# Kernel optimization log

Measured on AMD Instinct MI355X. Metric: run time of the kernel, lower is better.

## Reference

```python
import jax, jax.numpy as jnp
import numpy as np

B, S, H = 2, 2048, 1024
NH, NKV, HD = 16, 4, 64
G, R = NKV, NH // NKV  # 4 kv groups, 4 query heads per group


def setup_inputs() -> dict:
    key = jax.random.key(0)
    ks = jax.random.split(key, 7)
    scale = 1.0 / np.sqrt(H)
    return {
        "hidden_states": jax.random.normal(ks[0], (B, S, H), jnp.float32),
        "cos": jax.random.normal(ks[1], (S, HD), jnp.float32),
        "sin": jax.random.normal(ks[2], (S, HD), jnp.float32),
        "attention_mask": jnp.ones((B, S), jnp.float32),
        "Wq": jax.random.normal(ks[3], (H, NH * HD), jnp.float32) * scale,
        "Wk": jax.random.normal(ks[4], (H, NKV * HD), jnp.float32) * scale,
        "Wv": jax.random.normal(ks[5], (H, NKV * HD), jnp.float32) * scale,
        "Wo": jax.random.normal(ks[6], (NH * HD, H), jnp.float32) * scale,
    }


def _rotate_half(x):
    h = x.shape[-1] // 2
    return jnp.concatenate([-x[..., h:], x[..., :h]], axis=-1)


def reference(hidden_states, cos, sin, attention_mask, Wq, Wk, Wv, Wo):
    x = hidden_states
    q = (x @ Wq).reshape(B, S, NH, HD)
    k = (x @ Wk).reshape(B, S, NKV, HD)
    v = (x @ Wv).reshape(B, S, NKV, HD)
    # RoPE: cos/sin [S,HD] broadcast over batch and heads
    c = cos[None, :, None, :]
    s = sin[None, :, None, :]
    q = q * c + _rotate_half(q) * s
    k = k * c + _rotate_half(k) * s
    # GQA without materializing repeated KV: q grouped as [B,S,G,R,HD]
    qg = q.reshape(B, S, G, R, HD)
    scores = jnp.einsum("bsgrd,btgd->bgrst", qg, k) / np.sqrt(HD)  # [B,G,R,S,T]
    causal = jnp.tril(jnp.ones((S, S), bool))
    scores = jnp.where(causal[None, None, None], scores, -jnp.inf)
    scores = scores + ((1.0 - attention_mask) * -1e9)[:, None, None, None, :]
    probs = jax.nn.softmax(scores.astype(jnp.float32), axis=-1).astype(q.dtype)
    out = jnp.einsum("bgrst,btgd->bsgrd", probs, v).reshape(B, S, NH * HD)
    return out @ Wo
```

## Files before the change

kernel.cpp:

```cpp
#include <hip/hip_runtime.h>
#include <math.h>

#define B_   2
#define S_   2048
#define H_   1024
#define NH_  16
#define NKV_ 4
#define HD_  64
#define R_   (NH_ / NKV_)
#define QKVW 1536

typedef __attribute__((ext_vector_type(8))) short bf16x8;
typedef __attribute__((ext_vector_type(4))) float f32x4;

__device__ inline short f2bf(float f) {
    unsigned u = __float_as_uint(f);
    u += 0x7FFF + ((u >> 16) & 1);
    return (short)(u >> 16);
}

__device__ inline float exp2fast(float x) {
#if __has_builtin(__builtin_amdgcn_exp2f)
    return __builtin_amdgcn_exp2f(x);
#else
    float r; asm volatile("v_exp_f32 %0, %1\n\ts_nop 1" : "=v"(r) : "v"(x)); return r;
#endif
}

__device__ inline unsigned cvt_pk_bf16(float lo, float hi) {
    unsigned r;
    asm("v_cvt_pk_bf16_f32 %0, %1, %2" : "=v"(r) : "v"(lo), "v"(hi));
    return r;
}

#define LOG2E 1.4426950408889634f

__device__ inline void gload_lds16(const void* gptr, void* lptr) {
    __builtin_amdgcn_global_load_lds(
        (const __attribute__((address_space(1))) unsigned int*)gptr,
        (__attribute__((address_space(3))) unsigned int*)lptr,
        16, 0, 0);
}

__global__ __launch_bounds__(256) void tconv_all(const float* __restrict__ Wq,
                                                 const float* __restrict__ Wk,
                                                 const float* __restrict__ Wv,
                                                 const float* __restrict__ Wo,
                                                 short* __restrict__ Wqkvt,
                                                 short* __restrict__ Wot,
                                                 const float* __restrict__ x,
                                                 short* __restrict__ xb) {
    const int bx = blockIdx.x;
    const int tid = threadIdx.x;

    if (bx >= 640) {
        const size_t e0 = (size_t)(bx - 640) * 16384;
#pragma unroll
        for (int t = 0; t < 8; t++) {
            const size_t i = e0 + ((size_t)t * 256 + tid) * 8;
            float4 a = *(const float4*)&x[i];
            float4 c = *(const float4*)&x[i + 4];
            bf16x8 o;
            o[0] = f2bf(a.x); o[1] = f2bf(a.y); o[2] = f2bf(a.z); o[3] = f2bf(a.w);
            o[4] = f2bf(c.x); o[5] = f2bf(c.y); o[6] = f2bf(c.z); o[7] = f2bf(c.w);
            *(bf16x8*)&xb[i] = o;
        }
        return;
    }

    __shared__ short T[64][68];
    const float* W; short* Wt; int N, idx;
    if (bx < 256)      { W = Wq; Wt = Wqkvt;                     N = 1024; idx = bx; }
    else if (bx < 320) { W = Wk; Wt = Wqkvt + 1024 * 1024;       N = 256;  idx = bx - 256; }
    else if (bx < 384) { W = Wv; Wt = Wqkvt + 1280 * 1024;       N = 256;  idx = bx - 320; }
    else               { W = Wo; Wt = Wot;                       N = 1024; idx = bx - 384; }
    const int ntiles = N >> 6;
    const int n0 = (idx % ntiles) * 64;
    const int k0 = (idx / ntiles) * 64;

    const int r  = tid >> 4;
    const int c4 = (tid & 15) * 4;
#pragma unroll
    for (int t = 0; t < 4; t++) {
        int row = t * 16 + r;
        float4 v = *(const float4*)&W[(size_t)(k0 + row) * N + n0 + c4];
        T[c4 + 0][row] = f2bf(v.x);
        T[c4 + 1][row] = f2bf(v.y);
        T[c4 + 2][row] = f2bf(v.z);
        T[c4 + 3][row] = f2bf(v.w);
    }
    __syncthreads();
#pragma unroll
    for (int t = 0; t < 4; t++) {
        int row = t * 16 + r;
        short4 o = *(short4*)&T[row][c4];
        *(short4*)&Wt[(size_t)(n0 + row) * 1024 + k0 + c4] = o;
    }
}

__global__ __launch_bounds__(256) void gemm1_fused(const short* __restrict__ xb,
                                                   const short* __restrict__ Bt,
                                                   short* __restrict__ qkv,
                                                   short* __restrict__ Vtg,
                                                   const float* __restrict__ cosb,
                                                   const float* __restrict__ sinb) {
    __shared__ short Ah[2][64 * 32];
    __shared__ short Bh[2][128 * 32];

    const int tid  = threadIdx.x;
    const int w    = tid >> 6;
    const int lane = tid & 63;
    const int ln   = lane & 15;
    const int qd   = lane >> 4;
    const int wr   = w >> 1, wc = w & 1;
    const int row0 = blockIdx.y * 64;
    const int col0 = blockIdx.x * 128;

    const int sr = lane >> 2;
    const int sk = (lane & 3) * 8;

    const short* ap = xb + (size_t)(row0 + w * 16 + sr) * 1024 + sk;
    const short* bp0 = Bt + (size_t)(col0 + w * 32 + sr) * 1024 + sk;
    const short* bp1 = Bt + (size_t)(col0 + w * 32 + 16 + sr) * 1024 + sk;

    f32x4 acc[2][4];
#pragma unroll
    for (int mi = 0; mi < 2; mi++)
#pragma unroll
        for (int ni = 0; ni < 4; ni++)
            acc[mi][ni] = (f32x4){0.f, 0.f, 0.f, 0.f};

    gload_lds16(ap,  &Ah[0][(w * 16) * 32]);
    gload_lds16(bp0, &Bh[0][(w * 32) * 32]);
    gload_lds16(bp1, &Bh[0][(w * 32 + 16) * 32]);
    __syncthreads();

    for (int t = 0; t < 32; t++) {
        const int cur = t & 1, nxt = cur ^ 1;
        if (t + 1 < 32) {
            const int k1 = (t + 1) * 32;
            gload_lds16(ap + k1,  &Ah[nxt][(w * 16) * 32]);
            gload_lds16(bp0 + k1, &Bh[nxt][(w * 32) * 32]);
            gload_lds16(bp1 + k1, &Bh[nxt][(w * 32 + 16) * 32]);
        }

        bf16x8 af[2], bfr[4];
#pragma unroll
        for (int mi = 0; mi < 2; mi++)
            af[mi] = *(const bf16x8*)&Ah[cur][(wr * 32 + mi * 16 + ln) * 32 + qd * 8];
#pragma unroll
        for (int ni = 0; ni < 4; ni++)
            bfr[ni] = *(const bf16x8*)&Bh[cur][(wc * 64 + ni * 16 + ln) * 32 + qd * 8];
#pragma unroll
        for (int mi = 0; mi < 2; mi++)
#pragma unroll
            for (int ni = 0; ni < 4; ni++)
                acc[mi][ni] = __builtin_amdgcn_mfma_f32_16x16x32_bf16(af[mi], bfr[ni], acc[mi][ni], 0, 0, 0);

        __syncthreads();
    }

    const int colw = col0 + wc * 64;
    if (colw < H_ + NKV_ * HD_) {
#pragma unroll
        for (int mi = 0; mi < 2; mi++)
#pragma unroll
            for (int i = 0; i < 4; i++) {
                const int row  = row0 + wr * 32 + mi * 16 + qd * 4 + i;
                const int spos = row & (S_ - 1);
                const float* cp = cosb + (size_t)spos * HD_;
                const float* sp = sinb + (size_t)spos * HD_;
                float o0[4];
#pragma unroll
                for (int ni = 0; ni < 2; ni++) {
                    const int d = ni * 16 + ln;
                    float x0 = acc[mi][ni][i], x1 = acc[mi][ni + 2][i];
                    o0[ni]     = x0 * cp[d]      - x1 * sp[d];
                    o0[ni + 2] = x1 * cp[d + 32] + x0 * sp[d + 32];
                }
                short* Cp = qkv + (size_t)row * QKVW + colw + ln;
#pragma unroll
                for (int ni = 0; ni < 4; ni++) Cp[ni * 16] = f2bf(o0[ni]);
            }
    } else {
        const int g = (colw - (H_ + NKV_ * HD_)) >> 6;
#pragma unroll
        for (int mi = 0; mi < 2; mi++) {
            const int rbase = row0 + wr * 32 + mi * 16 + qd * 4;
            const int bg = ((rbase >> 11) * NKV_) + g;
            const int s0 = rbase & (S_ - 1);
#pragma unroll
            for (int ni = 0; ni < 4; ni++) {
                const int d = ni * 16 + ln;
                short4 pk = { f2bf(acc[mi][ni][0]), f2bf(acc[mi][ni][1]),
                              f2bf(acc[mi][ni][2]), f2bf(acc[mi][ni][3]) };
                *(short4*)&Vtg[((size_t)bg * HD_ + d) * S_ + s0] = pk;
            }
        }
    }
}

__global__ __launch_bounds__(256) void gemm2_bt(const short* __restrict__ A, int lda,
                                                const short* __restrict__ Bt,
                                                float* __restrict__ C, int ldc,
                                                int K) {
    __shared__ short Ah[2][64 * 32];
    __shared__ short Bh[2][128 * 32];

    const int tid  = threadIdx.x;
    const int w    = tid >> 6;
    const int lane = tid & 63;
    const int ln   = lane & 15;
    const int qd   = lane >> 4;
    const int wr   = w >> 1, wc = w & 1;
    const int row0 = blockIdx.y * 64;
    const int col0 = blockIdx.x * 128;

    const int sr = lane >> 2;
    const int sk = (lane & 3) * 8;

    const short* ap  = A + (size_t)(row0 + w * 16 + sr) * lda + sk;
    const short* bp0 = Bt + (size_t)(col0 + w * 32 + sr) * K + sk;
    const short* bp1 = Bt + (size_t)(col0 + w * 32 + 16 + sr) * K + sk;

    f32x4 acc[2][4];
#pragma unroll
    for (int mi = 0; mi < 2; mi++)
#pragma unroll
        for (int ni = 0; ni < 4; ni++)
            acc[mi][ni] = (f32x4){0.f, 0.f, 0.f, 0.f};

    const int nt = K >> 5;
    gload_lds16(ap,  &Ah[0][(w * 16) * 32]);
    gload_lds16(bp0, &Bh[0][(w * 32) * 32]);
    gload_lds16(bp1, &Bh[0][(w * 32 + 16) * 32]);
    __syncthreads();

    for (int t = 0; t < nt; t++) {
        const int cur = t & 1, nxt = cur ^ 1;
        if (t + 1 < nt) {
            const int k1 = (t + 1) * 32;
            gload_lds16(ap + k1,  &Ah[nxt][(w * 16) * 32]);
            gload_lds16(bp0 + k1, &Bh[nxt][(w * 32) * 32]);
            gload_lds16(bp1 + k1, &Bh[nxt][(w * 32 + 16) * 32]);
        }

        bf16x8 af[2], bfr[4];
#pragma unroll
        for (int mi = 0; mi < 2; mi++)
            af[mi] = *(const bf16x8*)&Ah[cur][(wr * 32 + mi * 16 + ln) * 32 + qd * 8];
#pragma unroll
        for (int ni = 0; ni < 4; ni++)
            bfr[ni] = *(const bf16x8*)&Bh[cur][(wc * 64 + ni * 16 + ln) * 32 + qd * 8];
#pragma unroll
        for (int mi = 0; mi < 2; mi++)
#pragma unroll
            for (int ni = 0; ni < 4; ni++)
                acc[mi][ni] = __builtin_amdgcn_mfma_f32_16x16x32_bf16(af[mi], bfr[ni], acc[mi][ni], 0, 0, 0);

        __syncthreads();
    }

#pragma unroll
    for (int mi = 0; mi < 2; mi++)
#pragma unroll
        for (int i = 0; i < 4; i++) {
            const size_t row = row0 + wr * 32 + mi * 16 + qd * 4 + i;
            float* Cp = C + row * ldc + col0 + wc * 64 + ln;
#pragma unroll
            for (int ni = 0; ni < 4; ni++) Cp[ni * 16] = acc[mi][ni][i];
        }
}

__global__ __launch_bounds__(512, 2) void attn_kernel(short* __restrict__ qkv,
                                                      const short* __restrict__ Vtg,
                                                      const float* __restrict__ maskb) {
    const int tid  = threadIdx.x;
    const int w    = tid >> 6;
    const int lane = tid & 63;
    const int ln   = lane & 15;
    const int qd   = lane >> 4;

    const int fid = blockIdx.x;
    const int bg  = fid & 7;
    const int u   = fid >> 3;
    const int b   = bg >> 2;
    const int g   = bg & 3;
    const int h   = g * R_ + (u & 3);
    const int a   = u >> 2;

    __shared__ short Ks[2][64 * 72];
    __shared__ short Vt[2][64 * 72];
    __shared__ short Ps[8][16 * 72];
    __shared__ float mskS[2][64];
    short* const ps = Ps[w];

    const short* const Kb = qkv + (size_t)b * S_ * QKVW + H_ + g * HD_;
    const short* const Vb = Vtg + (size_t)bg * HD_ * S_;
    const float* const mb = maskb + b * S_;

    const int fr = tid >> 3;
    const int fc = (tid & 7) * 8;

#pragma unroll 1
    for (int ph = 0; ph < 2; ph++) {
        const int qt   = ph ? (15 - a) : a;
        const int rowb = qt * 128 + w * 16;
        const int ktd  = 2 * qt + (w >> 2);
        const int ntp  = 2 * qt + 2;
        const int qrow = rowb + ln;

        bf16x8 qf0, qf1;
        {
            const short* qp = qkv + (size_t)(b * S_ + rowb + ln) * QKVW + h * HD_;
            qf0 = *(const bf16x8*)&qp[qd * 8];
            qf1 = *(const bf16x8*)&qp[32 + qd * 8];
        }

        f32x4 O[4] = {};
        float mrow = -1e30f, lrow = 0.0f;

        *(bf16x8*)&Ks[0][fr * 72 + fc] = *(const bf16x8*)&Kb[(size_t)fr * QKVW + fc];
        *(bf16x8*)&Vt[0][fr * 72 + fc] = *(const bf16x8*)&Vb[(size_t)fr * S_ + fc];
        if (tid < 64) mskS[0][tid] = (1.0f - mb[tid]) * (-1e9f * LOG2E);
        __syncthreads();

        int cur = 0;
#pragma unroll 1
        for (int kt = 0; kt < ntp; kt++) {
            const int base = kt * 64;
            const bool pf = (kt + 1 < ntp);

            bf16x8 pk, pv;
            float pm = 0.0f;
            if (pf) {
                const int nb = base + 64;
                pk = *(const bf16x8*)&Kb[(size_t)(nb + fr) * QKVW + fc];
                pv = *(const bf16x8*)&Vb[(size_t)fr * S_ + nb + fc];
                if (tid < 64) pm = (1.0f - mb[nb + tid]) * (-1e9f * LOG2E);
            }

            if (kt <= ktd) {
                f32x4 St[4];
#pragma unroll
                for (int kg = 0; kg < 4; kg++) {
                    bf16x8 ka0 = *(const bf16x8*)&Ks[cur][(kg * 16 + ln) * 72 + qd * 8];
                    bf16x8 ka1 = *(const bf16x8*)&Ks[cur][(kg * 16 + ln) * 72 + 32 + qd * 8];
                    f32x4 z = {0.f, 0.f, 0.f, 0.f};
                    z = __builtin_amdgcn_mfma_f32_16x16x32_bf16(ka0, qf0, z, 0, 0, 0);
                    St[kg] = __builtin_amdgcn_mfma_f32_16x16x32_bf16(ka1, qf1, z, 0, 0, 0);
                }

                bf16x8 vb[2][4];
#pragma unroll
                for (int kc2 = 0; kc2 < 2; kc2++)
#pragma unroll
                    for (int dt = 0; dt < 4; dt++)
                        vb[kc2][dt] = *(const bf16x8*)&Vt[cur][(dt * 16 + ln) * 72 + kc2 * 32 + qd * 8];

                float sc[4][4];
#pragma unroll
                for (int kg = 0; kg < 4; kg++) {
                    float4 mv = *(const float4*)&mskS[cur][kg * 16 + qd * 4];
                    sc[kg][0] = fmaf(St[kg][0], 0.125f * LOG2E, mv.x);
                    sc[kg][1] = fmaf(St[kg][1], 0.125f * LOG2E, mv.y);
                    sc[kg][2] = fmaf(St[kg][2], 0.125f * LOG2E, mv.z);
                    sc[kg][3] = fmaf(St[kg][3], 0.125f * LOG2E, mv.w);
                }
                if (kt == ktd) {
#pragma unroll
                    for (int kg = 0; kg < 4; kg++) {
                        const int keyb = base + kg * 16 + qd * 4;
#pragma unroll
                        for (int i = 0; i < 4; i++)
                            if (keyb + i > qrow) sc[kg][i] = -1e30f;
                    }
                }

                float mx = sc[0][0];
#pragma unroll
                for (int kg = 0; kg < 4; kg++)
#pragma unroll
                    for (int i = 0; i < 4; i++) mx = fmaxf(mx, sc[kg][i]);
                mx = fmaxf(mx, __shfl_xor(mx, 16));
                mx = fmaxf(mx, __shfl_xor(mx, 32));

                if (__ballot(mx > mrow + 11.5416f)) {
                    float nm    = fmaxf(mrow, mx);
                    float alpha = exp2fast(mrow - nm);
                    lrow *= alpha;
#pragma unroll
                    for (int i = 0; i < 4; i++) {
                        float av = __shfl(alpha, qd * 4 + i);
#pragma unroll
                        for (int dt = 0; dt < 4; dt++) O[dt][i] *= av;
                    }
                    mrow = nm;
                }
                const float nm = mrow;

                float ls = 0.0f;
#pragma unroll
                for (int kg = 0; kg < 4; kg++)
#pragma unroll
                    for (int i = 0; i < 4; i++) {
                        float p = exp2fast(sc[kg][i] - nm);
                        sc[kg][i] = p;
                        ls += p;
                    }
                ls += __shfl_xor(ls, 16);
                ls += __shfl_xor(ls, 32);
                lrow += ls;

#pragma unroll
                for (int kg = 0; kg < 4; kg++) {
                    uint2 pw;
                    pw.x = cvt_pk_bf16(sc[kg][0], sc[kg][1]);
                    pw.y = cvt_pk_bf16(sc[kg][2], sc[kg][3]);
                    *(uint2*)&ps[ln * 72 + kg * 16 + qd * 4] = pw;
                }

#pragma unroll
                for (int kc2 = 0; kc2 < 2; kc2++) {
                    bf16x8 pa = *(const bf16x8*)&ps[ln * 72 + kc2 * 32 + qd * 8];
#pragma unroll
                    for (int dt = 0; dt < 4; dt++)
                        O[dt] = __builtin_amdgcn_mfma_f32_16x16x32_bf16(pa, vb[kc2][dt], O[dt], 0, 0, 0);
                }
            }

            if (pf) {
                const int nxt = cur ^ 1;
                *(bf16x8*)&Ks[nxt][fr * 72 + fc] = pk;
                *(bf16x8*)&Vt[nxt][fr * 72 + fc] = pv;
                if (tid < 64) mskS[nxt][tid] = pm;
            }
            __syncthreads();
            cur ^= 1;
        }

#pragma unroll
        for (int i = 0; i < 4; i++) {
            float li  = __shfl(lrow, qd * 4 + i);
            float inv = 1.0f / li;
            const int row = rowb + qd * 4 + i;
            short* op = qkv + (size_t)(b * S_ + row) * QKVW + h * HD_ + ln;
#pragma unroll
            for (int dt = 0; dt < 4; dt++) op[dt * 16] = f2bf(O[dt][i] * inv);
        }
    }
}

extern "C" void kernel_launch(void* const* d_in, const int* in_sizes, int n_in,
                              void* d_out, int out_size, void* d_ws, size_t ws_size,
                              hipStream_t stream) {
    const float* x     = (const float*)d_in[0];
    const float* cosb  = (const float*)d_in[1];
    const float* sinb  = (const float*)d_in[2];
    const float* maskb = (const float*)d_in[3];
    const float* Wq    = (const float*)d_in[4];
    const float* Wk    = (const float*)d_in[5];
    const float* Wv    = (const float*)d_in[6];
    const float* Wo    = (const float*)d_in[7];

    const int M = B_ * S_;

    short* qkv   = (short*)d_ws;
    short* Wqkvt = qkv + (size_t)M * QKVW;
    short* Wot   = Wqkvt + (size_t)QKVW * H_;
    short* Vtg   = Wot + (size_t)H_ * H_;
    short* xb    = (short*)d_out;
    float* out   = (float*)d_out;

    dim3 blk(256);

    tconv_all<<<dim3(896), blk, 0, stream>>>(Wq, Wk, Wv, Wo, Wqkvt, Wot, x, xb);

    gemm1_fused<<<dim3(QKVW / 128, M / 64), blk, 0, stream>>>(xb, Wqkvt, qkv, Vtg, cosb, sinb);

    attn_kernel<<<dim3(256), dim3(512), 0, stream>>>(qkv, Vtg, maskb);

    gemm2_bt<<<dim3(H_ / 128, M / 64), blk, 0, stream>>>(qkv, QKVW, Wot, out, H_, H_);
}
```

Before: 183.7 us.

## Fuse x bf16 conversion into QKV GEMM and widen attention key tiles

Removes the separate fp32-to-bf16 pass over hidden_states: gemm1 now loads fp32 x directly, converts it in registers and writes it to LDS, in place of the async global-to-LDS copy. The attention kernel moves from 64-key to 128-key tiles with single-buffered LDS. It skips causally masked 16-key groups on the diagonal tile, reads the mask straight from global memory, and adds s_setprio around the MFMA sections. This cuts a kernel's worth of traffic and fewer loop iterations, at the cost of an extra barrier per tile, higher register pressure (launch bounds lowered to 1 block per CU), and a synchronous A-operand load path in gemm1.

```diff
diff --git a/kernel.cpp b/kernel.cpp
--- a/kernel.cpp
+++ b/kernel.cpp
@@ -47,28 +47,10 @@
                                                  const float* __restrict__ Wv,
                                                  const float* __restrict__ Wo,
                                                  short* __restrict__ Wqkvt,
-                                                 short* __restrict__ Wot,
-                                                 const float* __restrict__ x,
-                                                 short* __restrict__ xb) {
+                                                 short* __restrict__ Wot) {
+    __shared__ short T[64][68];
     const int bx = blockIdx.x;
     const int tid = threadIdx.x;
-
-    if (bx >= 640) {
-        const size_t e0 = (size_t)(bx - 640) * 16384;
-#pragma unroll
-        for (int t = 0; t < 8; t++) {
-            const size_t i = e0 + ((size_t)t * 256 + tid) * 8;
-            float4 a = *(const float4*)&x[i];
-            float4 c = *(const float4*)&x[i + 4];
-            bf16x8 o;
-            o[0] = f2bf(a.x); o[1] = f2bf(a.y); o[2] = f2bf(a.z); o[3] = f2bf(a.w);
-            o[4] = f2bf(c.x); o[5] = f2bf(c.y); o[6] = f2bf(c.z); o[7] = f2bf(c.w);
-            *(bf16x8*)&xb[i] = o;
-        }
-        return;
-    }
-
-    __shared__ short T[64][68];
     const float* W; short* Wt; int N, idx;
     if (bx < 256)      { W = Wq; Wt = Wqkvt;                     N = 1024; idx = bx; }
     else if (bx < 320) { W = Wk; Wt = Wqkvt + 1024 * 1024;       N = 256;  idx = bx - 256; }
@@ -98,7 +80,7 @@
     }
 }
 
-__global__ __launch_bounds__(256) void gemm1_fused(const short* __restrict__ xb,
+__global__ __launch_bounds__(256) void gemm1_fused(const float* __restrict__ x,
                                                    const short* __restrict__ Bt,
                                                    short* __restrict__ qkv,
                                                    short* __restrict__ Vtg,
@@ -118,8 +100,10 @@
 
     const int sr = lane >> 2;
     const int sk = (lane & 3) * 8;
-
-    const short* ap = xb + (size_t)(row0 + w * 16 + sr) * 1024 + sk;
+    const int ar  = tid >> 2;
+    const int ac8 = (tid & 3) * 8;
+
+    const float* xp  = x + (size_t)(row0 + ar) * 1024 + ac8;
     const short* bp0 = Bt + (size_t)(col0 + w * 32 + sr) * 1024 + sk;
     const short* bp1 = Bt + (size_t)(col0 + w * 32 + 16 + sr) * 1024 + sk;
 
@@ -130,7 +114,14 @@
         for (int ni = 0; ni < 4; ni++)
             acc[mi][ni] = (f32x4){0.f, 0.f, 0.f, 0.f};
 
-    gload_lds16(ap,  &Ah[0][(w * 16) * 32]);
+    {
+        float4 a1 = *(const float4*)xp;
+        float4 a2 = *(const float4*)(xp + 4);
+        bf16x8 o;
+        o[0]=f2bf(a1.x); o[1]=f2bf(a1.y); o[2]=f2bf(a1.z); o[3]=f2bf(a1.w);
+        o[4]=f2bf(a2.x); o[5]=f2bf(a2.y); o[6]=f2bf(a2.z); o[7]=f2bf(a2.w);
+        *(bf16x8*)&Ah[0][ar * 32 + ac8] = o;
+    }
     gload_lds16(bp0, &Bh[0][(w * 32) * 32]);
     gload_lds16(bp1, &Bh[0][(w * 32 + 16) * 32]);
     __syncthreads();
@@ -139,9 +130,14 @@
         const int cur = t & 1, nxt = cur ^ 1;
         if (t + 1 < 32) {
             const int k1 = (t + 1) * 32;
-            gload_lds16(ap + k1,  &Ah[nxt][(w * 16) * 32]);
             gload_lds16(bp0 + k1, &Bh[nxt][(w * 32) * 32]);
             gload_lds16(bp1 + k1, &Bh[nxt][(w * 32 + 16) * 32]);
+            float4 a1 = *(const float4*)(xp + k1);
+            float4 a2 = *(const float4*)(xp + k1 + 4);
+            bf16x8 o;
+            o[0]=f2bf(a1.x); o[1]=f2bf(a1.y); o[2]=f2bf(a1.z); o[3]=f2bf(a1.w);
+            o[4]=f2bf(a2.x); o[5]=f2bf(a2.y); o[6]=f2bf(a2.z); o[7]=f2bf(a2.w);
+            *(bf16x8*)&Ah[nxt][ar * 32 + ac8] = o;
         }
 
         bf16x8 af[2], bfr[4];
@@ -272,7 +268,7 @@
         }
 }
 
-__global__ __launch_bounds__(512, 2) void attn_kernel(short* __restrict__ qkv,
+__global__ __launch_bounds__(512, 1) void attn_kernel(short* __restrict__ qkv,
                                                       const short* __restrict__ Vtg,
                                                       const float* __restrict__ maskb) {
     const int tid  = threadIdx.x;
@@ -289,25 +285,25 @@
     const int h   = g * R_ + (u & 3);
     const int a   = u >> 2;
 
-    __shared__ short Ks[2][64 * 72];
-    __shared__ short Vt[2][64 * 72];
+    __shared__ short Ks[128 * 72];
+    __shared__ short Vt[64 * 136];
     __shared__ short Ps[8][16 * 72];
-    __shared__ float mskS[2][64];
     short* const ps = Ps[w];
 
     const short* const Kb = qkv + (size_t)b * S_ * QKVW + H_ + g * HD_;
     const short* const Vb = Vtg + (size_t)bg * HD_ * S_;
     const float* const mb = maskb + b * S_;
 
-    const int fr = tid >> 3;
-    const int fc = (tid & 7) * 8;
+    const int kr = tid >> 2;
+    const int kc = (tid & 3) * 16;
+    const int vr = tid >> 3;
+    const int vc = (tid & 7) * 16;
 
 #pragma unroll 1
     for (int ph = 0; ph < 2; ph++) {
         const int qt   = ph ? (15 - a) : a;
         const int rowb = qt * 128 + w * 16;
-        const int ktd  = 2 * qt + (w >> 2);
-        const int ntp  = 2 * qt + 2;
+        const int ntp  = qt + 1;
         const int qrow = rowb + ln;
 
         bf16x8 qf0, qf1;
@@ -320,123 +316,134 @@
         f32x4 O[4] = {};
         float mrow = -1e30f, lrow = 0.0f;
 
-        *(bf16x8*)&Ks[0][fr * 72 + fc] = *(const bf16x8*)&Kb[(size_t)fr * QKVW + fc];
-        *(bf16x8*)&Vt[0][fr * 72 + fc] = *(const bf16x8*)&Vb[(size_t)fr * S_ + fc];
-        if (tid < 64) mskS[0][tid] = (1.0f - mb[tid]) * (-1e9f * LOG2E);
+        *(bf16x8*)&Ks[kr * 72 + kc]      = *(const bf16x8*)&Kb[(size_t)kr * QKVW + kc];
+        *(bf16x8*)&Ks[kr * 72 + kc + 8]  = *(const bf16x8*)&Kb[(size_t)kr * QKVW + kc + 8];
+        *(bf16x8*)&Vt[vr * 136 + vc]     = *(const bf16x8*)&Vb[(size_t)vr * S_ + vc];
+        *(bf16x8*)&Vt[vr * 136 + vc + 8] = *(const bf16x8*)&Vb[(size_t)vr * S_ + vc + 8];
         __syncthreads();
 
-        int cur = 0;
 #pragma unroll 1
         for (int kt = 0; kt < ntp; kt++) {
-            const int base = kt * 64;
+            const int base = kt * 128;
             const bool pf = (kt + 1 < ntp);
 
-            bf16x8 pk, pv;
-            float pm = 0.0f;
+            bf16x8 pk0, pk1, pv0, pv1;
             if (pf) {
-                const int nb = base + 64;
-                pk = *(const bf16x8*)&Kb[(size_t)(nb + fr) * QKVW + fc];
-                pv = *(const bf16x8*)&Vb[(size_t)fr * S_ + nb + fc];
-                if (tid < 64) pm = (1.0f - mb[nb + tid]) * (-1e9f * LOG2E);
-            }
-
-            if (kt <= ktd) {
-                f32x4 St[4];
-#pragma unroll
-                for (int kg = 0; kg < 4; kg++) {
-                    bf16x8 ka0 = *(const bf16x8*)&Ks[cur][(kg * 16 + ln) * 72 + qd * 8];
-                    bf16x8 ka1 = *(const bf16x8*)&Ks[cur][(kg * 16 + ln) * 72 + 32 + qd * 8];
+                const int nb = base + 128;
+                pk0 = *(const bf16x8*)&Kb[(size_t)(nb + kr) * QKVW + kc];
+                pk1 = *(const bf16x8*)&Kb[(size_t)(nb + kr) * QKVW + kc + 8];
+                pv0 = *(const bf16x8*)&Vb[(size_t)vr * S_ + nb + vc];
+                pv1 = *(const bf16x8*)&Vb[(size_t)vr * S_ + nb + vc + 8];
+            }
+
+            const bool diag  = (kt == ntp - 1);
+            const int kgmax  = diag ? (w + 1) : 8;
+            const int c2max  = diag ? ((w >> 1) + 1) : 4;
+
+            f32x4 St[8];
+            __builtin_amdgcn_s_setprio(1);
+#pragma unroll
+            for (int kg = 0; kg < 8; kg++) {
+                if (kg < kgmax) {
+                    bf16x8 ka0 = *(const bf16x8*)&Ks[(kg * 16 + ln) * 72 + qd * 8];
+                    bf16x8 ka1 = *(const bf16x8*)&Ks[(kg * 16 + ln) * 72 + 32 + qd * 8];
                     f32x4 z = {0.f, 0.f, 0.f, 0.f};
                     z = __builtin_amdgcn_mfma_f32_16x16x32_bf16(ka0, qf0, z, 0, 0, 0);
                     St[kg] = __builtin_amdgcn_mfma_f32_16x16x32_bf16(ka1, qf1, z, 0, 0, 0);
                 }
-
-                bf16x8 vb[2][4];
-#pragma unroll
-                for (int kc2 = 0; kc2 < 2; kc2++)
-#pragma unroll
-                    for (int dt = 0; dt < 4; dt++)
-                        vb[kc2][dt] = *(const bf16x8*)&Vt[cur][(dt * 16 + ln) * 72 + kc2 * 32 + qd * 8];
-
-                float sc[4][4];
-#pragma unroll
-                for (int kg = 0; kg < 4; kg++) {
-                    float4 mv = *(const float4*)&mskS[cur][kg * 16 + qd * 4];
-                    sc[kg][0] = fmaf(St[kg][0], 0.125f * LOG2E, mv.x);
-                    sc[kg][1] = fmaf(St[kg][1], 0.125f * LOG2E, mv.y);
-                    sc[kg][2] = fmaf(St[kg][2], 0.125f * LOG2E, mv.z);
-                    sc[kg][3] = fmaf(St[kg][3], 0.125f * LOG2E, mv.w);
-                }
-                if (kt == ktd) {
-#pragma unroll
-                    for (int kg = 0; kg < 4; kg++) {
-                        const int keyb = base + kg * 16 + qd * 4;
-#pragma unroll
-                        for (int i = 0; i < 4; i++)
-                            if (keyb + i > qrow) sc[kg][i] = -1e30f;
+            }
+            __builtin_amdgcn_s_setprio(0);
+
+            const float MX = 1e9f * LOG2E;
+#pragma unroll
+            for (int kg = 0; kg < 8; kg++) {
+                float4 mv = *(const float4*)&mb[base + kg * 16 + qd * 4];
+                St[kg][0] = fmaf(St[kg][0], 0.125f * LOG2E, fmaf(mv.x, MX, -MX));
+                St[kg][1] = fmaf(St[kg][1], 0.125f * LOG2E, fmaf(mv.y, MX, -MX));
+                St[kg][2] = fmaf(St[kg][2], 0.125f * LOG2E, fmaf(mv.z, MX, -MX));
+                St[kg][3] = fmaf(St[kg][3], 0.125f * LOG2E, fmaf(mv.w, MX, -MX));
+            }
+            if (diag) {
+#pragma unroll
+                for (int kg = 0; kg < 8; kg++) {
+                    const int keyb = base + kg * 16 + qd * 4;
+#pragma unroll
+                    for (int i = 0; i < 4; i++)
+                        if (keyb + i > qrow) St[kg][i] = -1e30f;
+                }
+            }
+
+            float mx = St[0][0];
+#pragma unroll
+            for (int kg = 0; kg < 8; kg++)
+#pragma unroll
+                for (int i = 0; i < 4; i++) mx = fmaxf(mx, St[kg][i]);
+            mx = fmaxf(mx, __shfl_xor(mx, 16));
+            mx = fmaxf(mx, __shfl_xor(mx, 32));
+
+            if (__ballot(mx > mrow + 11.5416f)) {
+                float nm    = fmaxf(mrow, mx);
+                float alpha = exp2fast(mrow - nm);
+                lrow *= alpha;
+#pragma unroll
+                for (int i = 0; i < 4; i++) {
+                    float av = __shfl(alpha, qd * 4 + i);
+#pragma unroll
+                    for (int dt = 0; dt < 4; dt++) O[dt][i] *= av;
+                }
+                mrow = nm;
+            }
+            const float nm = mrow;
+
+            float ls = 0.0f;
+#pragma unroll
+            for (int kg = 0; kg < 8; kg++)
+#pragma unroll
+                for (int i = 0; i < 4; i++) {
+                    float p = exp2fast(St[kg][i] - nm);
+                    St[kg][i] = p;
+                    ls += p;
+                }
+            ls += __shfl_xor(ls, 16);
+            ls += __shfl_xor(ls, 32);
+            lrow += ls;
+
+            __builtin_amdgcn_s_setprio(1);
+#pragma unroll
+            for (int hh = 0; hh < 2; hh++) {
+                if (hh * 2 < c2max) {
+#pragma unroll
+                    for (int k4 = 0; k4 < 4; k4++) {
+                        const int kg = hh * 4 + k4;
+                        uint2 pw;
+                        pw.x = cvt_pk_bf16(St[kg][0], St[kg][1]);
+                        pw.y = cvt_pk_bf16(St[kg][2], St[kg][3]);
+                        *(uint2*)&ps[ln * 72 + k4 * 16 + qd * 4] = pw;
                     }
-                }
-
-                float mx = sc[0][0];
-#pragma unroll
-                for (int kg = 0; kg < 4; kg++)
-#pragma unroll
-                    for (int i = 0; i < 4; i++) mx = fmaxf(mx, sc[kg][i]);
-                mx = fmaxf(mx, __shfl_xor(mx, 16));
-                mx = fmaxf(mx, __shfl_xor(mx, 32));
-
-                if (__ballot(mx > mrow + 11.5416f)) {
-                    float nm    = fmaxf(mrow, mx);
-                    float alpha = exp2fast(mrow - nm);
-                    lrow *= alpha;
-#pragma unroll
-                    for (int i = 0; i < 4; i++) {
-                        float av = __shfl(alpha, qd * 4 + i);
-#pragma unroll
-                        for (int dt = 0; dt < 4; dt++) O[dt][i] *= av;
+#pragma unroll
+                    for (int c2 = 0; c2 < 2; c2++) {
+                        const int kc2 = hh * 2 + c2;
+                        if (kc2 < c2max) {
+                            bf16x8 pa = *(const bf16x8*)&ps[ln * 72 + c2 * 32 + qd * 8];
+#pragma unroll
+                            for (int dt = 0; dt < 4; dt++) {
+                                bf16x8 vb = *(const bf16x8*)&Vt[(dt * 16 + ln) * 136 + kc2 * 32 + qd * 8];
+                                O[dt] = __builtin_amdgcn_mfma_f32_16x16x32_bf16(pa, vb, O[dt], 0, 0, 0);
+                            }
+                        }
                     }
-                    mrow = nm;
-                }
-                const float nm = mrow;
-
-                float ls = 0.0f;
-#pragma unroll
-                for (int kg = 0; kg < 4; kg++)
-#pragma unroll
-                    for (int i = 0; i < 4; i++) {
-                        float p = exp2fast(sc[kg][i] - nm);
-                        sc[kg][i] = p;
-                        ls += p;
-                    }
-                ls += __shfl_xor(ls, 16);
-                ls += __shfl_xor(ls, 32);
-                lrow += ls;
-
-#pragma unroll
-                for (int kg = 0; kg < 4; kg++) {
-                    uint2 pw;
-                    pw.x = cvt_pk_bf16(sc[kg][0], sc[kg][1]);
-                    pw.y = cvt_pk_bf16(sc[kg][2], sc[kg][3]);
-                    *(uint2*)&ps[ln * 72 + kg * 16 + qd * 4] = pw;
-                }
-
-#pragma unroll
-                for (int kc2 = 0; kc2 < 2; kc2++) {
-                    bf16x8 pa = *(const bf16x8*)&ps[ln * 72 + kc2 * 32 + qd * 8];
-#pragma unroll
-                    for (int dt = 0; dt < 4; dt++)
-                        O[dt] = __builtin_amdgcn_mfma_f32_16x16x32_bf16(pa, vb[kc2][dt], O[dt], 0, 0, 0);
-                }
-            }
-
+                }
+            }
+            __builtin_amdgcn_s_setprio(0);
+
+            __syncthreads();
             if (pf) {
-                const int nxt = cur ^ 1;
-                *(bf16x8*)&Ks[nxt][fr * 72 + fc] = pk;
-                *(bf16x8*)&Vt[nxt][fr * 72 + fc] = pv;
-                if (tid < 64) mskS[nxt][tid] = pm;
+                *(bf16x8*)&Ks[kr * 72 + kc]      = pk0;
+                *(bf16x8*)&Ks[kr * 72 + kc + 8]  = pk1;
+                *(bf16x8*)&Vt[vr * 136 + vc]     = pv0;
+                *(bf16x8*)&Vt[vr * 136 + vc + 8] = pv1;
             }
             __syncthreads();
-            cur ^= 1;
         }
 
 #pragma unroll
@@ -469,14 +476,13 @@
     short* Wqkvt = qkv + (size_t)M * QKVW;
     short* Wot   = Wqkvt + (size_t)QKVW * H_;
     short* Vtg   = Wot + (size_t)H_ * H_;
-    short* xb    = (short*)d_out;
     float* out   = (float*)d_out;
 
     dim3 blk(256);
 
-    tconv_all<<<dim3(896), blk, 0, stream>>>(Wq, Wk, Wv, Wo, Wqkvt, Wot, x, xb);
-
-    gemm1_fused<<<dim3(QKVW / 128, M / 64), blk, 0, stream>>>(xb, Wqkvt, qkv, Vtg, cosb, sinb);
+    tconv_all<<<dim3(640), blk, 0, stream>>>(Wq, Wk, Wv, Wo, Wqkvt, Wot);
+
+    gemm1_fused<<<dim3(QKVW / 128, M / 64), blk, 0, stream>>>(x, Wqkvt, qkv, Vtg, cosb, sinb);
 
     attn_kernel<<<dim3(256), dim3(512), 0, stream>>>(qkv, Vtg, maskb);
 
```

Measured after the change: 193.0 us. 1.05x slower.
